# Kernel optimization log

Measured on AMD Instinct MI355X. Metric: run time of the kernel, lower is better.

Reference implementation:

```python
import jax, jax.numpy as jnp
import numpy as np

K = 7            # kernel_size
PAD = 3          # (dilation*(K-1)+1)//2
SHARE = 8        # share_planes
CIN = 512; REL = 64; COUT = 512
B = 4; H = 32; W = 32
EPS = 1e-5


def _patches(x, k, pad):
    """Reflect-pad then extract kxk local windows.
    x: [B,C,H,W] -> [B, C, k*k, H*W] (row-major kernel-offset ordering,
    matching torch Unfold / SAN's Subtraction ordering)."""
    b, c, h, w = x.shape
    xp = jnp.pad(x, ((0, 0), (0, 0), (pad, pad), (pad, pad)), mode='reflect')
    pats = jnp.stack([xp[:, :, i:i + h, j:j + w]
                      for i in range(k) for j in range(k)], axis=2)
    return pats.reshape(b, c, k * k, h * w)


def setup_inputs() -> dict:
    key = jax.random.key(0)
    ks = jax.random.split(key, 16)
    n = lambda k_, shp, s=0.05: jax.random.normal(k_, shp, dtype=jnp.float32) * s
    return {
        'x': jax.random.normal(ks[0], (B, CIN, H, W), dtype=jnp.float32),
        # 1x1 query/key/value projections
        'w1': n(ks[1], (REL, CIN)), 'b1': n(ks[2], (REL,)),
        'w2': n(ks[3], (REL, CIN)), 'b2': n(ks[4], (REL,)),
        'w3': n(ks[5], (COUT, CIN)), 'b3': n(ks[6], (COUT,)),
        # conv_p: 1x1 conv on 2-channel position map
        'wp': n(ks[7], (2, 2), 0.5), 'bp': n(ks[8], (2,)),
        # conv_w: BN(rel+2) -> ReLU -> 1x1(rel+2->rel, no bias) -> BN(rel) -> ReLU -> 1x1(rel->out/share)
        'g0': jnp.ones((REL + 2,), jnp.float32), 'be0': jnp.zeros((REL + 2,), jnp.float32),
        'm0': n(ks[9], (REL + 2,), 0.1),
        'v0': jax.random.uniform(ks[10], (REL + 2,), jnp.float32, 0.5, 1.5),
        'wcw1': n(ks[11], (REL, REL + 2)),
        'g1': jnp.ones((REL,), jnp.float32), 'be1': jnp.zeros((REL,), jnp.float32),
        'm1': n(ks[12], (REL,), 0.1),
        'v1': jax.random.uniform(ks[13], (REL,), jnp.float32, 0.5, 1.5),
        'wcw2': n(ks[14], (COUT // SHARE, REL)), 'bcw2': n(ks[15], (COUT // SHARE,)),
    }


def reference(x, w1, b1, w2, b2, w3, b3, wp, bp,
              g0, be0, m0, v0, wcw1, g1, be1, m1, v1, wcw2, bcw2):
    b, c, h, w = x.shape
    hw = h * w
    conv1x1 = lambda W_, B_, t: jnp.einsum('oc,bchw->bohw', W_, t) + B_[None, :, None, None]
    bn = lambda t, g, be, m, v: ((t - m[None, :, None, None])
                                 * (g * jax.lax.rsqrt(v + EPS))[None, :, None, None]
                                 + be[None, :, None, None])

    x1 = conv1x1(w1, b1, x)   # [B,REL,H,W]
    x2 = conv1x1(w2, b2, x)   # [B,REL,H,W]
    x3 = conv1x1(w3, b3, x)   # [B,COUT,H,W]

    # position map: channel 0 = loc_w, channel 1 = loc_h (as in source)
    lw = jnp.broadcast_to(jnp.linspace(-1.0, 1.0, w)[None, :], (h, w))
    lh = jnp.broadcast_to(jnp.linspace(-1.0, 1.0, h)[:, None], (h, w))
    p = jnp.stack([lw, lh])[None].astype(x.dtype)          # [1,2,H,W]
    p = jnp.einsum('oc,bchw->bohw', wp, p) + bp[None, :, None, None]

    # Subtraction2(x1, x2): center query minus key neighbors -> [B,REL,K*K,HW]
    sub2 = x1.reshape(b, REL, 1, hw) - _patches(x2, K, PAD)
    # Subtraction(p): center minus neighbors -> [1,2,K*K,HW], repeat over batch
    subp = p.reshape(1, 2, 1, hw) - _patches(p, K, PAD)
    subp = jnp.broadcast_to(subp, (b, 2, K * K, hw))

    t = jnp.concatenate([sub2, subp], axis=1)              # [B,REL+2,K*K,HW]
    t = jax.nn.relu(bn(t, g0, be0, m0, v0))
    t = jnp.einsum('oc,bckn->bokn', wcw1, t)               # [B,REL,K*K,HW]
    t = jax.nn.relu(bn(t, g1, be1, m1, v1))
    wgt = jnp.einsum('oc,bckn->bokn', wcw2, t) + bcw2[None, :, None, None]
    wgt = jax.nn.softmax(wgt, axis=-2)                     # softmax over K*K window dim

    # Aggregation: out[b,c,n] = sum_k wgt[b, c//SHARE, k, n] * x3_patch[b,c,k,n]
    x3p = _patches(x3, K, PAD).reshape(b, COUT // SHARE, SHARE, K * K, hw)
    out = jnp.einsum('bgskn,bgkn->bgsn', x3p, wgt)
    return out.reshape(b, COUT, h, w)
```

## Files before the change

### kernel.cpp

```cpp
#include <hip/hip_runtime.h>
#include <hip/hip_bf16.h>
#include <math.h>

typedef float f32x4 __attribute__((ext_vector_type(4)));
typedef short s16x8 __attribute__((ext_vector_type(8)));

#define KKW 49
#define HWTOT 1024
#define CIN 512
#define COUT 512

#define OFF_X1T 0
#define OFF_X2T 262144
#define OFF_X3T 524288
#define OFF_PM  2621440
#define OFF_A0  2623488
#define OFF_C0  2623554
#define OFF_W64 2623620
#define OFF_W65 2623684
#define OFF_C1V 2623748
#define OFF_W1B 2623812
#define OFF_W2B 2625860
#define OFF_W2F 2627908
#define OFF_WT  2629956
#define OFF_XT  2793796
#define WS_NEED_FLOATS 3842372ull

#define SWZ(bb)  ((bb) ^ ((((bb) >> 7) & 7) << 4))

#define GLD16(g, l) __builtin_amdgcn_global_load_lds( \
    (const __attribute__((address_space(1))) void*)(g), \
    (__attribute__((address_space(3))) void*)(l), 16, 0, 0)

__device__ __forceinline__ int refl(int m) {
    if (m < 0) m = -m;
    if (m > 31) m = 62 - m;
    return m;
}

__device__ __forceinline__ unsigned short fbf(float f) {
    unsigned u = __builtin_bit_cast(unsigned, f);
    unsigned r = u + 0x7fffu + ((u >> 16) & 1u);
    return (unsigned short)(r >> 16);
}

__device__ __forceinline__ unsigned pk2bf(float a, float b) {
    float2 f2; f2.x = a; f2.y = b;
    __hip_bfloat162 h = __float22bfloat162_rn(f2);
    union { __hip_bfloat162 h2; unsigned u; } cv;
    cv.h2 = h;
    return cv.u;
}

__device__ __forceinline__ float bf2f(unsigned short u) {
    unsigned v = (unsigned)u << 16;
    return __builtin_bit_cast(float, v);
}

__global__ void k_setup(const float* __restrict__ wp, const float* __restrict__ bp,
                        const float* __restrict__ g0, const float* __restrict__ be0,
                        const float* __restrict__ m0, const float* __restrict__ v0,
                        const float* __restrict__ wcw1,
                        const float* __restrict__ g1, const float* __restrict__ be1,
                        const float* __restrict__ m1, const float* __restrict__ v1,
                        const float* __restrict__ wcw2,
                        float* __restrict__ ws) {
    int tid = threadIdx.x;
    float* pm = ws + OFF_PM;
    for (int n = tid; n < HWTOT; n += 256) {
        int xx = n & 31, yy = n >> 5;
        float lw = -1.f + (2.f / 31.f) * xx;
        float lh = -1.f + (2.f / 31.f) * yy;
        pm[n * 2 + 0] = wp[0] * lw + wp[1] * lh + bp[0];
        pm[n * 2 + 1] = wp[2] * lw + wp[3] * lh + bp[1];
    }
    if (tid < 66) {
        float a = g0[tid] * rsqrtf(v0[tid] + 1e-5f);
        ws[OFF_A0 + tid] = a;
        ws[OFF_C0 + tid] = be0[tid] - m0[tid] * a;
    }
    if (tid < 64) {
        float a1c = g1[tid] * rsqrtf(v1[tid] + 1e-5f);
        ws[OFF_W64 + tid] = a1c * wcw1[tid * 66 + 64];
        ws[OFF_W65 + tid] = a1c * wcw1[tid * 66 + 65];
        ws[OFF_C1V + tid] = be1[tid] - m1[tid] * a1c;
    }
    unsigned short* w1b = (unsigned short*)(ws + OFF_W1B);
    unsigned short* w2f = (unsigned short*)(ws + OFF_W2F);
    for (int t = tid; t < 4096; t += 256) {
        int co = t >> 6, r = t & 63;
        float a1c = g1[co] * rsqrtf(v1[co] + 1e-5f);
        w1b[t] = fbf(a1c * wcw1[co * 66 + r]);
        int j = t & 7, idx = t >> 3;
        int ft = idx >> 6, l = idx & 63;
        int gt = ft >> 1, ks2 = ft & 1;
        int g = (l & 15) + gt * 16;
        int c2 = ks2 * 32 + (l >> 4) * 8 + j;
        w2f[t] = fbf(wcw2[g * 64 + c2]);
    }
}

__global__ __launch_bounds__(256) void k_prep(
        const float* __restrict__ x,
        const float* __restrict__ w1, const float* __restrict__ w2,
        const float* __restrict__ w3, float* __restrict__ ws) {
    int bid = blockIdx.x;
    int tid = threadIdx.x;
    if (bid < 40) {
        int mT = bid / 8, kT = bid % 8;
        char* dst = (char*)(ws + OFF_WT) + (mT * 8 + kT) * 16384;
#pragma unroll
        for (int it = 0; it < 4; ++it) {
            int item = it * 256 + tid;
            int m = item >> 3, k8 = item & 7;
            int mg = mT * 128 + m;
            const float* src;
            if (mg < 64) src = w1 + mg * CIN;
            else if (mg < 128) src = w2 + (mg - 64) * CIN;
            else src = w3 + (mg - 128) * CIN;
            int k0 = kT * 64 + k8 * 8;
            s16x8 h;
#pragma unroll
            for (int i = 0; i < 8; i++) h[i] = (short)fbf(src[k0 + i]);
            *(s16x8*)(dst + SWZ(m * 128 + k8 * 16)) = h;
        }
    } else {
        __shared__ float lds[64 * 129];
        int t = bid - 40;
        int b = t >> 6, nT = (t >> 3) & 7, kT = t & 7;
        const float* src = x + (b * CIN + kT * 64) * HWTOT + nT * 128;
#pragma unroll
        for (int it = 0; it < 8; ++it) {
            int item = it * 256 + tid;
            int kk = item >> 5, n4 = item & 31;
            float4 v = *(const float4*)(src + kk * HWTOT + n4 * 4);
            float* d = &lds[kk * 129 + n4 * 4];
            d[0] = v.x; d[1] = v.y; d[2] = v.z; d[3] = v.w;
        }
        __syncthreads();
        char* dst = (char*)(ws + OFF_XT) + ((b * 8 + nT) * 8 + kT) * 16384;
#pragma unroll
        for (int it = 0; it < 4; ++it) {
            int item = it * 256 + tid;
            int n = item >> 3, k8 = item & 7;
            s16x8 h;
#pragma unroll
            for (int i = 0; i < 8; i++) h[i] = (short)fbf(lds[(k8 * 8 + i) * 129 + n]);
            *(s16x8*)(dst + SWZ(n * 128 + k8 * 16)) = h;
        }
    }
}

__global__ __launch_bounds__(256) void k_projm(
        const float* __restrict__ b1, const float* __restrict__ b2,
        const float* __restrict__ b3, float* __restrict__ ws) {
    __shared__ __align__(16) char smem[65536];
    int tid = threadIdx.x, lane = tid & 63, wv = tid >> 6;
    int lidx = lane & 15, q = lane >> 4;
    int mT = blockIdx.x, nT = blockIdx.y, b = blockIdx.z;
    int mh = wv >> 1, nh = wv & 1;
    const char* wtg = (const char*)(ws + OFF_WT) + mT * 8 * 16384;
    const char* xtg = (const char*)(ws + OFF_XT) + (b * 8 + nT) * 8 * 16384;

    f32x4 acc[4][4];
#pragma unroll
    for (int i = 0; i < 4; i++)
#pragma unroll
        for (int j = 0; j < 4; j++) acc[i][j] = (f32x4)0.f;

#define STAGE(kt, buf) do { \
        const char* ga_ = wtg + (kt) * 16384; \
        const char* gb_ = xtg + (kt) * 16384; \
        char* la_ = smem + (buf) * 32768; \
        char* lb_ = la_ + 16384; \
        _Pragma("unroll") \
        for (int c_ = 0; c_ < 4; c_++) { \
            GLD16(ga_ + c_ * 4096 + wv * 1024 + lane * 16, la_ + c_ * 4096 + wv * 1024); \
            GLD16(gb_ + c_ * 4096 + wv * 1024 + lane * 16, lb_ + c_ * 4096 + wv * 1024); \
        } \
    } while (0)

    STAGE(0, 0);
    __syncthreads();
    for (int kt = 0; kt < 8; kt++) {
        if (kt < 7) STAGE(kt + 1, (kt + 1) & 1);
        const char* la = smem + (kt & 1) * 32768;
        const char* lb = la + 16384;
#pragma unroll
        for (int ks = 0; ks < 2; ks++) {
            s16x8 af[4], bf[4];
            int kb = ks * 64 + q * 16;
#pragma unroll
            for (int f = 0; f < 4; f++) {
                int arow = mh * 64 + f * 16 + lidx;
                int brow = nh * 64 + f * 16 + lidx;
                af[f] = *(const s16x8*)(la + SWZ(arow * 128 + kb));
                bf[f] = *(const s16x8*)(lb + SWZ(brow * 128 + kb));
            }
#pragma unroll
            for (int mf = 0; mf < 4; mf++)
#pragma unroll
                for (int nf = 0; nf < 4; nf++)
                    acc[mf][nf] = __builtin_amdgcn_mfma_f32_16x16x32_bf16(
                        af[mf], bf[nf], acc[mf][nf], 0, 0, 0);
        }
        __syncthreads();
    }
#undef STAGE

    unsigned short* x1t = (unsigned short*)(ws + OFF_X1T);
    unsigned short* x2t = (unsigned short*)(ws + OFF_X2T);
    unsigned short* x3t = (unsigned short*)(ws + OFF_X3T);
#pragma unroll
    for (int mf = 0; mf < 4; mf++) {
        int mloc = mh * 64 + mf * 16 + q * 4;
        int mg = mT * 128 + mloc;
#pragma unroll
        for (int nf = 0; nf < 4; nf++) {
            int n = nT * 128 + nh * 64 + nf * 16 + lidx;
            float o[4];
            uint2 pk;
            if (mg < 64) {
#pragma unroll
                for (int r = 0; r < 4; r++)
                    o[r] = ws[OFF_A0 + mg + r] * (acc[mf][nf][r] + b1[mg + r]) + ws[OFF_C0 + mg + r];
                pk.x = pk2bf(o[0], o[1]); pk.y = pk2bf(o[2], o[3]);
                *(uint2*)(x1t + (size_t)(b * HWTOT + n) * 64 + mg) = pk;
            } else if (mg < 128) {
                int c = mg - 64;
#pragma unroll
                for (int r = 0; r < 4; r++)
                    o[r] = ws[OFF_A0 + c + r] * (acc[mf][nf][r] + b2[c + r]);
                pk.x = pk2bf(o[0], o[1]); pk.y = pk2bf(o[2], o[3]);
                *(uint2*)(x2t + (size_t)(b * HWTOT + n) * 64 + c) = pk;
            } else {
                int c = mg - 128;
#pragma unroll
                for (int r = 0; r < 4; r++)
                    o[r] = acc[mf][nf][r] + b3[c + r];
                pk.x = pk2bf(o[0], o[1]); pk.y = pk2bf(o[2], o[3]);
                *(uint2*)(x3t + (size_t)(b * HWTOT + n) * 512 + c) = pk;
            }
        }
    }
}

__global__ __launch_bounds__(256) void k_proj(
        const float* __restrict__ x,
        const float* __restrict__ w1, const float* __restrict__ b1,
        const float* __restrict__ w2, const float* __restrict__ b2,
        const float* __restrict__ w3, const float* __restrict__ b3,
        float* __restrict__ ws) {
    __shared__ __align__(16) float As[64 * 17];
    __shared__ __align__(16) float Bs[16 * 64];
    int tid = threadIdx.x;
    int n0 = blockIdx.x * 64;
    int mT = blockIdx.y;
    int b = blockIdx.z;
    int mq = tid >> 4, nq = tid & 15;
    float acc[4][4];
#pragma unroll
    for (int i = 0; i < 4; i++)
#pragma unroll
        for (int j = 0; j < 4; j++) acc[i][j] = 0.f;

    for (int k0 = 0; k0 < CIN; k0 += 16) {
#pragma unroll
        for (int i = 0; i < 4; i++) {
            int t = tid + i * 256;
            int k = t & 15, m = t >> 4;
            int mg = mT * 64 + m;
            const float* Wrow;
            if (mg < 64) Wrow = w1 + mg * CIN;
            else if (mg < 128) Wrow = w2 + (mg - 64) * CIN;
            else Wrow = w3 + (mg - 128) * CIN;
            As[m * 17 + k] = Wrow[k0 + k];
        }
#pragma unroll
        for (int i = 0; i < 4; i++) {
            int t = tid + i * 256;
            int n = t & 63, k = t >> 6;
            Bs[k * 64 + n] = x[(b * CIN + k0 + k) * HWTOT + n0 + n];
        }
        __syncthreads();
#pragma unroll
        for (int k = 0; k < 16; k++) {
            float4 bv = *(const float4*)&Bs[k * 64 + nq * 4];
            float av[4];
#pragma unroll
            for (int i = 0; i < 4; i++) av[i] = As[(mq * 4 + i) * 17 + k];
#pragma unroll
            for (int i = 0; i < 4; i++) {
                acc[i][0] += av[i] * bv.x;
                acc[i][1] += av[i] * bv.y;
                acc[i][2] += av[i] * bv.z;
                acc[i][3] += av[i] * bv.w;
            }
        }
        __syncthreads();
    }
    unsigned short* x1t = (unsigned short*)(ws + OFF_X1T);
    unsigned short* x2t = (unsigned short*)(ws + OFF_X2T);
    unsigned short* x3t = (unsigned short*)(ws + OFF_X3T);
#pragma unroll
    for (int i = 0; i < 4; i++) {
        int mg = mT * 64 + mq * 4 + i;
        if (mg < 64) {
            float bias = b1[mg];
            float aa = ws[OFF_A0 + mg], cc = ws[OFF_C0 + mg];
#pragma unroll
            for (int j = 0; j < 4; j++) {
                int n = n0 + nq * 4 + j;
                x1t[(size_t)(b * HWTOT + n) * 64 + mg] = fbf(aa * (acc[i][j] + bias) + cc);
            }
        } else if (mg < 128) {
            int r = mg - 64;
            float bias = b2[r];
            float aa = ws[OFF_A0 + r];
#pragma unroll
            for (int j = 0; j < 4; j++) {
                int n = n0 + nq * 4 + j;
                x2t[(size_t)(b * HWTOT + n) * 64 + r] = fbf(aa * (acc[i][j] + bias));
            }
        } else {
            float bias = b3[mg - 128];
#pragma unroll
            for (int j = 0; j < 4; j++) {
                int n = n0 + nq * 4 + j;
                x3t[(size_t)(b * HWTOT + n) * 512 + (mg - 128)] = fbf(acc[i][j] + bias);
            }
        }
    }
}

__global__ __launch_bounds__(256, 4) void k_fused(
        const float* __restrict__ ws, float* __restrict__ out) {
    __shared__ __align__(16) char smem[35840];

    int tid = threadIdx.x;
    int lane = tid & 63;
    int wv = tid >> 6;
    int lidx = lane & 15;
    int q = lane >> 4;

    int bid = blockIdx.x;
    int gsw = (bid & 7) * 128 + (bid >> 3);
    int p = gsw * 4 + wv;
    int b = p >> 10;
    int n = p & 1023;
    int y = n >> 5, x0 = n & 31;

    char* t1p = smem + wv * 8960;
    float* auxf = (float*)(smem + wv * 8960 + 8192);
    int* nbo = (int*)(smem + wv * 8960 + 8704);

    const unsigned short* x1t = (const unsigned short*)(ws + OFF_X1T);
    const unsigned short* x2t = (const unsigned short*)(ws + OFF_X2T);
    const unsigned short* x3t = (const unsigned short*)(ws + OFF_X3T);
    const float* pm  = ws + OFF_PM;
    const unsigned short* w1b = (const unsigned short*)(ws + OFF_W1B);
    const unsigned short* w2f = (const unsigned short*)(ws + OFF_W2F);

    {
        int k = lane;
        int di = k / 7 - 3, dj = k % 7 - 3;
        int nb = refl(y + di) * 32 + refl(x0 + dj);
        nbo[k] = nb;
        float a064 = ws[OFF_A0 + 64], c064 = ws[OFF_C0 + 64];
        float a065 = ws[OFF_A0 + 65], c065 = ws[OFF_C0 + 65];
        auxf[k]      = fmaxf(fmaf(a064, pm[n * 2 + 0] - pm[nb * 2 + 0], c064), 0.f);
        auxf[64 + k] = fmaxf(fmaf(a065, pm[n * 2 + 1] - pm[nb * 2 + 1], c065), 0.f);
    }
    __syncthreads();

    s16x8 af1[4][2];
#pragma unroll
    for (int cot = 0; cot < 4; cot++)
#pragma unroll
        for (int ks = 0; ks < 2; ks++)
            af1[cot][ks] = *(const s16x8*)(w1b + (lidx + 16 * cot) * 64 + ks * 32 + q * 8);

    const unsigned short* x1r = x1t + (size_t)(b * HWTOT + n) * 64 + q * 8;
    float x1f[2][8];
    {
        s16x8 h0 = *(const s16x8*)(x1r);
        s16x8 h1 = *(const s16x8*)(x1r + 32);
#pragma unroll
        for (int i = 0; i < 8; i++) {
            x1f[0][i] = bf2f((unsigned short)h0[i]);
            x1f[1][i] = bf2f((unsigned short)h1[i]);
        }
    }

#pragma unroll
    for (int ct = 0; ct < 4; ct++) {
        int col = lidx + 16 * ct;
        int nb = nbo[col];
        const unsigned short* x2r = x2t + (size_t)(b * HWTOT + nb) * 64 + q * 8;
        f32x4 acc1[4];
#pragma unroll
        for (int cot = 0; cot < 4; cot++) acc1[cot] = (f32x4)0.f;
#pragma unroll
        for (int ks = 0; ks < 2; ks++) {
            s16x8 v = *(const s16x8*)(x2r + ks * 32);
            union { s16x8 v; unsigned u[4]; } bb;
#pragma unroll
            for (int w = 0; w < 4; w++)
                bb.u[w] = pk2bf(
                    fmaxf(x1f[ks][2 * w]     - bf2f((unsigned short)v[2 * w]),     0.f),
                    fmaxf(x1f[ks][2 * w + 1] - bf2f((unsigned short)v[2 * w + 1]), 0.f));
#pragma unroll
            for (int cot = 0; cot < 4; cot++)
                acc1[cot] = __builtin_amdgcn_mfma_f32_16x16x32_bf16(af1[cot][ks], bb.v, acc1[cot], 0, 0, 0);
        }
        float s64 = auxf[col], s65 = auxf[64 + col];
#pragma unroll
        for (int cot = 0; cot < 4; cot++) {
            f32x4 wa = *(const f32x4*)(ws + OFF_W64 + cot * 16 + q * 4);
            f32x4 wb = *(const f32x4*)(ws + OFF_W65 + cot * 16 + q * 4);
            f32x4 cc = *(const f32x4*)(ws + OFF_C1V + cot * 16 + q * 4);
            float t[4];
#pragma unroll
            for (int r = 0; r < 4; r++)
                t[r] = fmaxf(acc1[cot][r] + wa[r] * s64 + wb[r] * s65 + cc[r], 0.f);
            uint2 pk;
            pk.x = pk2bf(t[0], t[1]);
            pk.y = pk2bf(t[2], t[3]);
            int byte = col * 128 + cot * 32 + q * 8;
            *(uint2*)(t1p + SWZ(byte)) = pk;
        }
    }

    asm volatile("s_waitcnt lgkmcnt(0)" ::: "memory");
    __builtin_amdgcn_sched_barrier(0);

    s16x8 af2[4][2];
#pragma unroll
    for (int gt = 0; gt < 4; gt++)
#pragma unroll
        for (int ks2 = 0; ks2 < 2; ks2++)
            af2[gt][ks2] = *(const s16x8*)(w2f + ((gt * 2 + ks2) * 64 + lane) * 8);

    unsigned held[4][4][2];
#pragma unroll
    for (int gt = 0; gt < 4; gt++) {
        f32x4 acc2[4];
#pragma unroll
        for (int kt = 0; kt < 4; kt++) acc2[kt] = (f32x4)0.f;
#pragma unroll
        for (int kt = 0; kt < 4; kt++) {
#pragma unroll
            for (int ks2 = 0; ks2 < 2; ks2++) {
                int byte = (lidx + 16 * kt) * 128 + ks2 * 64 + q * 16;
                s16x8 a = *(const s16x8*)(t1p + SWZ(byte));
                acc2[kt] = __builtin_amdgcn_mfma_f32_16x16x32_bf16(a, af2[gt][ks2], acc2[kt], 0, 0, 0);
            }
        }
        float mx = -1e30f;
#pragma unroll
        for (int kt = 0; kt < 3; kt++)
#pragma unroll
            for (int r = 0; r < 4; r++) mx = fmaxf(mx, acc2[kt][r]);
        if (q == 0) mx = fmaxf(mx, acc2[3][0]);
        mx = fmaxf(mx, __shfl_xor(mx, 16));
        mx = fmaxf(mx, __shfl_xor(mx, 32));
        float e[4][4];
        float sum = 0.f;
#pragma unroll
        for (int kt = 0; kt < 4; kt++)
#pragma unroll
            for (int r = 0; r < 4; r++) {
                bool valid = (kt < 3) || (q == 0 && r == 0);
                float ev = valid ? exp2f((acc2[kt][r] - mx) * 1.44269504f) : 0.f;
                e[kt][r] = ev;
                sum += ev;
            }
        sum += __shfl_xor(sum, 16);
        sum += __shfl_xor(sum, 32);
        float inv = 1.f / sum;
#pragma unroll
        for (int kt = 0; kt < 4; kt++) {
            held[gt][kt][0] = pk2bf(e[kt][0] * inv, e[kt][1] * inv);
            held[gt][kt][1] = pk2bf(e[kt][2] * inv, e[kt][3] * inv);
        }
    }

#pragma unroll
    for (int gt = 0; gt < 4; gt++)
#pragma unroll
        for (int kt = 0; kt < 4; kt++) {
            int byte = (lidx + 16 * gt) * 128 + kt * 32 + q * 8;
            uint2 pk;
            pk.x = held[gt][kt][0];
            pk.y = held[gt][kt][1];
            *(uint2*)(t1p + SWZ(byte)) = pk;
        }

    asm volatile("s_waitcnt lgkmcnt(0)" ::: "memory");
    __builtin_amdgcn_sched_barrier(0);

    s16x8 wrow[7];
#pragma unroll
    for (int i = 0; i < 7; i++)
        wrow[i] = *(const s16x8*)(t1p + SWZ(lane * 128 + i * 16));

    f32x4 a30 = (f32x4)0.f, a31 = (f32x4)0.f;
    const unsigned short* x3b = x3t + (size_t)b * HWTOT * 512 + lane * 8;
#pragma unroll
    for (int k = 0; k < KKW; k++) {
        int nb = nbo[k];
        float w = bf2f((unsigned short)wrow[k >> 3][k & 7]);
        s16x8 v = *(const s16x8*)(x3b + (size_t)nb * 512);
#pragma unroll
        for (int r = 0; r < 4; r++) {
            a30[r] = fmaf(w, bf2f((unsigned short)v[r]), a30[r]);
            a31[r] = fmaf(w, bf2f((unsigned short)v[4 + r]), a31[r]);
        }
    }
    float* ob = out + ((size_t)b * COUT + lane * 8) * HWTOT + n;
#pragma unroll
    for (int i = 0; i < 4; i++) ob[i * HWTOT] = a30[i];
#pragma unroll
    for (int i = 0; i < 4; i++) ob[(i + 4) * HWTOT] = a31[i];
}

extern "C" void kernel_launch(void* const* d_in, const int* in_sizes, int n_in,
                              void* d_out, int out_size, void* d_ws, size_t ws_size,
                              hipStream_t stream) {
    const float* x = (const float*)d_in[0];
    const float* w1 = (const float*)d_in[1];
    const float* b1 = (const float*)d_in[2];
    const float* w2 = (const float*)d_in[3];
    const float* b2 = (const float*)d_in[4];
    const float* w3 = (const float*)d_in[5];
    const float* b3 = (const float*)d_in[6];
    const float* wp = (const float*)d_in[7];
    const float* bp = (const float*)d_in[8];
    const float* g0 = (const float*)d_in[9];
    const float* be0 = (const float*)d_in[10];
    const float* m0 = (const float*)d_in[11];
    const float* v0 = (const float*)d_in[12];
    const float* wcw1 = (const float*)d_in[13];
    const float* g1 = (const float*)d_in[14];
    const float* be1 = (const float*)d_in[15];
    const float* m1 = (const float*)d_in[16];
    const float* v1 = (const float*)d_in[17];
    const float* wcw2 = (const float*)d_in[18];
    float* ws = (float*)d_ws;
    float* out = (float*)d_out;

    k_setup<<<1, 256, 0, stream>>>(wp, bp, g0, be0, m0, v0, wcw1, g1, be1, m1, v1, wcw2, ws);
    if (ws_size >= WS_NEED_FLOATS * 4ull) {
        k_prep<<<296, 256, 0, stream>>>(x, w1, w2, w3, ws);
        k_projm<<<dim3(5, 8, 4), 256, 0, stream>>>(b1, b2, b3, ws);
    } else {
        k_proj<<<dim3(16, 10, 4), 256, 0, stream>>>(x, w1, b1, w2, b2, w3, b3, ws);
    }
    k_fused<<<1024, 256, 0, stream>>>(ws, out);
}
```

Baseline: 65.41 us.

## Fold setup into prep launch and run fused kernel as single-wave blocks

The one-block setup kernel becomes an extra block (index 296) of the prep kernel, removing one launch in the main path. The fused kernel changes from 256-thread blocks of four independent waves to 64-thread single-wave blocks (4096 blocks). This lets the block barrier be replaced by an LDS wait plus a scheduling barrier, and each wave can retire independently. The costs are more blocks to schedule, a different pixel-to-block swizzle, and a launch_bounds occupancy hint that now applies per wave.

Result: faster. 62.33 us (-4.7%).

```diff
diff --git a/kernel.cpp b/kernel.cpp
--- a/kernel.cpp
+++ b/kernel.cpp
@@ -57,15 +57,16 @@
     return __builtin_bit_cast(float, v);
 }
 
-__global__ void k_setup(const float* __restrict__ wp, const float* __restrict__ bp,
-                        const float* __restrict__ g0, const float* __restrict__ be0,
-                        const float* __restrict__ m0, const float* __restrict__ v0,
-                        const float* __restrict__ wcw1,
-                        const float* __restrict__ g1, const float* __restrict__ be1,
-                        const float* __restrict__ m1, const float* __restrict__ v1,
-                        const float* __restrict__ wcw2,
-                        float* __restrict__ ws) {
-    int tid = threadIdx.x;
+__device__ __forceinline__ void setup_body(
+        int tid,
+        const float* __restrict__ wp, const float* __restrict__ bp,
+        const float* __restrict__ g0, const float* __restrict__ be0,
+        const float* __restrict__ m0, const float* __restrict__ v0,
+        const float* __restrict__ wcw1,
+        const float* __restrict__ g1, const float* __restrict__ be1,
+        const float* __restrict__ m1, const float* __restrict__ v1,
+        const float* __restrict__ wcw2,
+        float* __restrict__ ws) {
     float* pm = ws + OFF_PM;
     for (int n = tid; n < HWTOT; n += 256) {
         int xx = n & 31, yy = n >> 5;
@@ -100,13 +101,34 @@
     }
 }
 
+__global__ void k_setup(const float* __restrict__ wp, const float* __restrict__ bp,
+                        const float* __restrict__ g0, const float* __restrict__ be0,
+                        const float* __restrict__ m0, const float* __restrict__ v0,
+                        const float* __restrict__ wcw1,
+                        const float* __restrict__ g1, const float* __restrict__ be1,
+                        const float* __restrict__ m1, const float* __restrict__ v1,
+                        const float* __restrict__ wcw2,
+                        float* __restrict__ ws) {
+    setup_body(threadIdx.x, wp, bp, g0, be0, m0, v0, wcw1, g1, be1, m1, v1, wcw2, ws);
+}
+
 __global__ __launch_bounds__(256) void k_prep(
         const float* __restrict__ x,
         const float* __restrict__ w1, const float* __restrict__ w2,
-        const float* __restrict__ w3, float* __restrict__ ws) {
+        const float* __restrict__ w3,
+        const float* __restrict__ wp, const float* __restrict__ bp,
+        const float* __restrict__ g0, const float* __restrict__ be0,
+        const float* __restrict__ m0, const float* __restrict__ v0,
+        const float* __restrict__ wcw1,
+        const float* __restrict__ g1, const float* __restrict__ be1,
+        const float* __restrict__ m1, const float* __restrict__ v1,
+        const float* __restrict__ wcw2,
+        float* __restrict__ ws) {
     int bid = blockIdx.x;
     int tid = threadIdx.x;
-    if (bid < 40) {
+    if (bid == 296) {
+        setup_body(tid, wp, bp, g0, be0, m0, v0, wcw1, g1, be1, m1, v1, wcw2, ws);
+    } else if (bid < 40) {
         int mT = bid / 8, kT = bid % 8;
         char* dst = (char*)(ws + OFF_WT) + (mT * 8 + kT) * 16384;
 #pragma unroll
@@ -333,26 +355,23 @@
     }
 }
 
-__global__ __launch_bounds__(256, 4) void k_fused(
+__global__ __launch_bounds__(64, 4) void k_fused(
         const float* __restrict__ ws, float* __restrict__ out) {
-    __shared__ __align__(16) char smem[35840];
-
-    int tid = threadIdx.x;
-    int lane = tid & 63;
-    int wv = tid >> 6;
+    __shared__ __align__(16) char smem[8960];
+
+    int lane = threadIdx.x;
     int lidx = lane & 15;
     int q = lane >> 4;
 
     int bid = blockIdx.x;
-    int gsw = (bid & 7) * 128 + (bid >> 3);
-    int p = gsw * 4 + wv;
+    int p = (bid & 7) * 512 + (bid >> 3);
     int b = p >> 10;
     int n = p & 1023;
     int y = n >> 5, x0 = n & 31;
 
-    char* t1p = smem + wv * 8960;
-    float* auxf = (float*)(smem + wv * 8960 + 8192);
-    int* nbo = (int*)(smem + wv * 8960 + 8704);
+    char* t1p = smem;
+    float* auxf = (float*)(smem + 8192);
+    int* nbo = (int*)(smem + 8704);
 
     const unsigned short* x1t = (const unsigned short*)(ws + OFF_X1T);
     const unsigned short* x2t = (const unsigned short*)(ws + OFF_X2T);
@@ -371,7 +390,8 @@
         auxf[k]      = fmaxf(fmaf(a064, pm[n * 2 + 0] - pm[nb * 2 + 0], c064), 0.f);
         auxf[64 + k] = fmaxf(fmaf(a065, pm[n * 2 + 1] - pm[nb * 2 + 1], c065), 0.f);
     }
-    __syncthreads();
+    asm volatile("s_waitcnt lgkmcnt(0)" ::: "memory");
+    __builtin_amdgcn_sched_barrier(0);
 
     s16x8 af1[4][2];
 #pragma unroll
@@ -549,12 +569,13 @@
     float* ws = (float*)d_ws;
     float* out = (float*)d_out;
 
-    k_setup<<<1, 256, 0, stream>>>(wp, bp, g0, be0, m0, v0, wcw1, g1, be1, m1, v1, wcw2, ws);
     if (ws_size >= WS_NEED_FLOATS * 4ull) {
-        k_prep<<<296, 256, 0, stream>>>(x, w1, w2, w3, ws);
+        k_prep<<<297, 256, 0, stream>>>(x, w1, w2, w3, wp, bp, g0, be0, m0, v0,
+                                        wcw1, g1, be1, m1, v1, wcw2, ws);
         k_projm<<<dim3(5, 8, 4), 256, 0, stream>>>(b1, b2, b3, ws);
     } else {
+        k_setup<<<1, 256, 0, stream>>>(wp, bp, g0, be0, m0, v0, wcw1, g1, be1, m1, v1, wcw2, ws);
         k_proj<<<dim3(16, 10, 4), 256, 0, stream>>>(x, w1, b1, w2, b2, w3, b3, ws);
     }
-    k_fused<<<1024, 256, 0, stream>>>(ws, out);
-}
+    k_fused<<<4096, 64, 0, stream>>>(ws, out);
+}
```
